# Kernel optimization log

Hardware: AMD Instinct MI355X
Metric: run time of the kernel (lower is better)

The kernel has to match this reference:

```python
import jax, jax.numpy as jnp
import numpy as np

N_NODES = 50000

def _gcn_layer(h, src, dst, norm, W, activate):
    # symmetric-normalized aggregation: D^-1/2 A D^-1/2 h, then linear
    h = h * norm[:, None]                      # [N, d] pre-scale
    msg = h[src]                               # gather over edges [E, d]
    agg = jax.ops.segment_sum(msg, dst, num_segments=N_NODES)  # scatter-add
    h = agg * norm[:, None]                    # post-scale
    h = h @ W
    return jax.nn.relu(h) if activate else h


def setup_inputs() -> dict:
    key = jax.random.key(0)
    k1, k2, k3, k4, k5, k6 = jax.random.split(key, 6)
    d_in, d_hid, d_out, n_edges = 128, 128, 40, 640000
    features = jax.random.normal(k1, (N_NODES, d_in), dtype=jnp.float32)
    edge_index = jax.random.randint(k2, (2, n_edges), 0, N_NODES, dtype=jnp.int64)
    s = 1.0 / np.sqrt(d_hid)
    W0 = jax.random.normal(k3, (d_in, d_hid), dtype=jnp.float32) * s
    W1 = jax.random.normal(k4, (d_hid, d_hid), dtype=jnp.float32) * s
    W2 = jax.random.normal(k5, (d_hid, d_hid), dtype=jnp.float32) * s
    W3 = jax.random.normal(k6, (d_hid, d_out), dtype=jnp.float32) * s
    return {"features": features, "edge_index": edge_index,
            "W0": W0, "W1": W1, "W2": W2, "W3": W3}


def reference(features, edge_index, W0, W1, W2, W3):
    src, dst = edge_index[0], edge_index[1]
    # in-degree based symmetric norm (graph_norm=True), clamp isolated nodes
    deg = jax.ops.segment_sum(jnp.ones_like(dst, dtype=features.dtype), dst,
                              num_segments=N_NODES)
    norm = jax.lax.rsqrt(jnp.maximum(deg, 1.0))
    h = features
    h = _gcn_layer(h, src, dst, norm, W0, True)
    h = _gcn_layer(h, src, dst, norm, W1, True)
    h = _gcn_layer(h, src, dst, norm, W2, True)
    h = _gcn_layer(h, src, dst, norm, W3, False)  # last layer: no activation
    return h
```

## Files before the change

### kernel.cpp

```cpp
#include <hip/hip_runtime.h>
#include <hip/hip_fp16.h>


#define DIM 128
#define CHUNK 1024

typedef __attribute__((ext_vector_type(8))) _Float16 f16x8;
typedef __attribute__((ext_vector_type(4))) float f32x4;

__global__ void deg_kernel(const int* __restrict__ dst, int* __restrict__ deg, int E) {
    int i = blockIdx.x * blockDim.x + threadIdx.x;
    if (i < E) atomicAdd(&deg[dst[i]], 1);
}

__global__ __launch_bounds__(256) void scanA_kernel(
        const int* __restrict__ deg, float* __restrict__ nrm,
        int* __restrict__ bsum, int n) {
    int b = blockIdx.x, t = threadIdx.x;
    int base = b * CHUNK + t * 4;
    int s = 0;
    if (base + 3 < n) {
        int4 d = *(const int4*)&deg[base];
        s = d.x + d.y + d.z + d.w;
        float4 r;
        r.x = rsqrtf(fmaxf((float)d.x, 1.0f));
        r.y = rsqrtf(fmaxf((float)d.y, 1.0f));
        r.z = rsqrtf(fmaxf((float)d.z, 1.0f));
        r.w = rsqrtf(fmaxf((float)d.w, 1.0f));
        *(float4*)&nrm[base] = r;
    } else {
        for (int j = 0; j < 4; ++j) {
            int idx = base + j;
            if (idx < n) {
                int d = deg[idx];
                s += d;
                nrm[idx] = rsqrtf(fmaxf((float)d, 1.0f));
            }
        }
    }
    for (int o = 32; o; o >>= 1) s += __shfl_down(s, o, 64);
    __shared__ int ws[4];
    if ((t & 63) == 0) ws[t >> 6] = s;
    __syncthreads();
    if (t == 0) bsum[b] = ws[0] + ws[1] + ws[2] + ws[3];
}

__global__ __launch_bounds__(256) void scanBC_kernel(
        const int* __restrict__ deg, const int* __restrict__ bsum,
        int* __restrict__ off, int* __restrict__ cur, int n, int G) {
    __shared__ int pbs;
    __shared__ int wsum[4];
    int b = blockIdx.x, t = threadIdx.x;
    if (t < 64) {
        int orig = (t < G) ? bsum[t] : 0;
        int v = orig;
        for (int o = 1; o < 64; o <<= 1) {
            int u = __shfl_up(v, o, 64);
            if (t >= o) v += u;
        }
        if (b == 0 && t == G - 1) off[n] = v;
        if (t == b) pbs = v - orig;
    }
    int base = b * CHUNK + t * 4;
    if (base + 3 < n) *(int4*)&cur[base] = make_int4(0, 0, 0, 0);
    else for (int j = 0; j < 4; ++j) if (base + j < n) cur[base + j] = 0;

    int d0 = 0, d1 = 0, d2 = 0, d3 = 0;
    if (base + 3 < n) {
        int4 d = *(const int4*)&deg[base];
        d0 = d.x; d1 = d.y; d2 = d.z; d3 = d.w;
    } else {
        if (base     < n) d0 = deg[base];
        if (base + 1 < n) d1 = deg[base + 1];
        if (base + 2 < n) d2 = deg[base + 2];
    }
    int tot = d0 + d1 + d2 + d3;
    int v = tot;
    for (int o = 1; o < 64; o <<= 1) {
        int u = __shfl_up(v, o, 64);
        if ((t & 63) >= o) v += u;
    }
    if ((t & 63) == 63) wsum[t >> 6] = v;
    __syncthreads();
    int wbase = 0;
    for (int w = 0; w < (t >> 6); ++w) wbase += wsum[w];
    int p = pbs + wbase + (v - tot);
    if (base + 3 < n) {
        int4 o4 = make_int4(p, p + d0, p + d0 + d1, p + d0 + d1 + d2);
        *(int4*)&off[base] = o4;
    } else {
        if (base     < n) off[base]     = p;
        if (base + 1 < n) off[base + 1] = p + d0;
        if (base + 2 < n) off[base + 2] = p + d0 + d1;
    }
}

__global__ void fill_kernel(const int* __restrict__ src, const int* __restrict__ dst,
                            const int* __restrict__ off, int* __restrict__ cur,
                            int* __restrict__ csr, int E) {
    int i = blockIdx.x * blockDim.x + threadIdx.x;
    if (i < E) {
        int d = dst[i];
        int p = atomicAdd(&cur[d], 1);
        csr[off[d] + p] = src[i];
    }
}

__global__ void conv_kernel(const float* __restrict__ f, const float* __restrict__ nrm,
                            __half* __restrict__ out, int n4) {
    int i = blockIdx.x * blockDim.x + threadIdx.x;
    if (i < n4) {
        int r = i >> 5, c4 = i & 31;
        float s = nrm[r];
        float4 v = ((const float4*)f)[i];
        __half2 lo = __float22half2_rn(make_float2(v.x * s, v.y * s));
        __half2 hi = __float22half2_rn(make_float2(v.z * s, v.w * s));
        uint2 u;
        u.x = *(unsigned int*)&lo;
        u.y = *(unsigned int*)&hi;
        *(uint2*)&out[(size_t)r * DIM + c4 * 4] = u;
    }
}

__global__ void convW_kernel(const float* __restrict__ W0, const float* __restrict__ W1,
                             const float* __restrict__ W2, const float* __restrict__ W3,
                             __half* __restrict__ Wt) {
    int i = blockIdx.x * blockDim.x + threadIdx.x;
    if (i < 3 * 128 * 128) {
        int l = i >> 14;
        int c = (i >> 7) & 127, k = i & 127;
        const float* W = (l == 0) ? W0 : ((l == 1) ? W1 : W2);
        Wt[i] = __float2half(W[k * 128 + c]);
    } else if (i < 3 * 128 * 128 + 48 * 128) {
        int j = i - 3 * 128 * 128;
        int c = j >> 7, k = j & 127;
        Wt[i] = __float2half((c < 40) ? W3[k * 40 + c] : 0.f);
    }
}

__global__ __launch_bounds__(256) void aggh_kernel(
        const __half* __restrict__ hin, const float* __restrict__ nrm,
        const int* __restrict__ off, const int* __restrict__ csr,
        __half* __restrict__ out, int N) {
    int t = threadIdx.x;
    int lane = t & 63;
    int node = blockIdx.x * 4 + (t >> 6);
    if (node >= N) return;
    int pos = lane & 15, sg = lane >> 4;
    int c = pos * 8;
    int b = off[node], e = off[node + 1];
    float a[8] = {0,0,0,0,0,0,0,0};
    float bb[8] = {0,0,0,0,0,0,0,0};
    int j = b + sg;
    for (; j + 4 < e; j += 8) {
        int s0 = csr[j], s1 = csr[j + 4];
        uint4 u0 = *(const uint4*)&hin[(size_t)s0 * DIM + c];
        uint4 u1 = *(const uint4*)&hin[(size_t)s1 * DIM + c];
        float2 f;
        f = __half22float2(*(__half2*)&u0.x); a[0]+=f.x; a[1]+=f.y;
        f = __half22float2(*(__half2*)&u0.y); a[2]+=f.x; a[3]+=f.y;
        f = __half22float2(*(__half2*)&u0.z); a[4]+=f.x; a[5]+=f.y;
        f = __half22float2(*(__half2*)&u0.w); a[6]+=f.x; a[7]+=f.y;
        f = __half22float2(*(__half2*)&u1.x); bb[0]+=f.x; bb[1]+=f.y;
        f = __half22float2(*(__half2*)&u1.y); bb[2]+=f.x; bb[3]+=f.y;
        f = __half22float2(*(__half2*)&u1.z); bb[4]+=f.x; bb[5]+=f.y;
        f = __half22float2(*(__half2*)&u1.w); bb[6]+=f.x; bb[7]+=f.y;
    }
    for (; j < e; j += 4) {
        uint4 u = *(const uint4*)&hin[(size_t)csr[j] * DIM + c];
        float2 f;
        f = __half22float2(*(__half2*)&u.x); a[0]+=f.x; a[1]+=f.y;
        f = __half22float2(*(__half2*)&u.y); a[2]+=f.x; a[3]+=f.y;
        f = __half22float2(*(__half2*)&u.z); a[4]+=f.x; a[5]+=f.y;
        f = __half22float2(*(__half2*)&u.w); a[6]+=f.x; a[7]+=f.y;
    }
#pragma unroll
    for (int k = 0; k < 8; ++k) a[k] += bb[k];
#pragma unroll
    for (int k = 0; k < 8; ++k) {
        a[k] += __shfl_xor(a[k], 16, 64);
        a[k] += __shfl_xor(a[k], 32, 64);
    }
    if (sg == 0) {
        float s = nrm[node];
        __half2 h0 = __float22half2_rn(make_float2(a[0]*s, a[1]*s));
        __half2 h1 = __float22half2_rn(make_float2(a[2]*s, a[3]*s));
        __half2 h2 = __float22half2_rn(make_float2(a[4]*s, a[5]*s));
        __half2 h3 = __float22half2_rn(make_float2(a[6]*s, a[7]*s));
        uint4 u;
        u.x = *(unsigned int*)&h0; u.y = *(unsigned int*)&h1;
        u.z = *(unsigned int*)&h2; u.w = *(unsigned int*)&h3;
        *(uint4*)&out[(size_t)node * DIM + c] = u;
    }
}

__global__ __launch_bounds__(256) void gemmM_kernel(
        const __half* __restrict__ Ah, const __half* __restrict__ Wt,
        const float* __restrict__ nrm, __half* __restrict__ outh, int n) {
    int t = threadIdx.x;
    int lane = t & 63, wv = t >> 6;
    int row0 = blockIdx.x * 64 + wv * 16;
    int arow = row0 + (lane & 15);
    int ar = (arow < n) ? arow : (n - 1);
    int kg = lane >> 4;

    const __half* Abase = Ah + (size_t)ar * DIM + kg * 8;
    f16x8 a[4];
#pragma unroll
    for (int k0 = 0; k0 < 4; ++k0)
        a[k0] = *(const f16x8*)(Abase + k0 * 32);

    f32x4 acc[8];
#pragma unroll
    for (int ct = 0; ct < 8; ++ct) {
        acc[ct] = (f32x4){0.f, 0.f, 0.f, 0.f};
        const __half* Bbase = Wt + (size_t)(ct * 16 + (lane & 15)) * DIM + kg * 8;
#pragma unroll
        for (int k0 = 0; k0 < 4; ++k0) {
            f16x8 b = *(const f16x8*)(Bbase + k0 * 32);
            acc[ct] = __builtin_amdgcn_mfma_f32_16x16x32_f16(a[k0], b, acc[ct], 0, 0, 0);
        }
    }

    int col = lane & 15;
    int rbase = row0 + (lane >> 4) * 4;
#pragma unroll
    for (int r = 0; r < 4; ++r) {
        int row = rbase + r;
        if (row >= n) continue;
        float s = nrm[row];
#pragma unroll
        for (int ct = 0; ct < 8; ++ct) {
            float v = fmaxf(acc[ct][r], 0.f) * s;
            outh[(size_t)row * DIM + ct * 16 + col] = __float2half(v);
        }
    }
}

__global__ __launch_bounds__(256) void gemm3M_kernel(
        const __half* __restrict__ Ah, const __half* __restrict__ Wt3,
        __half* __restrict__ outh, int n) {
    int t = threadIdx.x;
    int lane = t & 63, wv = t >> 6;
    int row0 = blockIdx.x * 64 + wv * 16;
    int arow = row0 + (lane & 15);
    int ar = (arow < n) ? arow : (n - 1);
    int kg = lane >> 4;

    const __half* Abase = Ah + (size_t)ar * DIM + kg * 8;
    f16x8 a[4];
#pragma unroll
    for (int k0 = 0; k0 < 4; ++k0)
        a[k0] = *(const f16x8*)(Abase + k0 * 32);

    f32x4 acc[3];
#pragma unroll
    for (int ct = 0; ct < 3; ++ct) {
        acc[ct] = (f32x4){0.f, 0.f, 0.f, 0.f};
        const __half* Bbase = Wt3 + (size_t)(ct * 16 + (lane & 15)) * DIM + kg * 8;
#pragma unroll
        for (int k0 = 0; k0 < 4; ++k0) {
            f16x8 b = *(const f16x8*)(Bbase + k0 * 32);
            acc[ct] = __builtin_amdgcn_mfma_f32_16x16x32_f16(a[k0], b, acc[ct], 0, 0, 0);
        }
    }

    int col = lane & 15;
    int rbase = row0 + (lane >> 4) * 4;
#pragma unroll
    for (int r = 0; r < 4; ++r) {
        int row = rbase + r;
        if (row >= n) continue;
#pragma unroll
        for (int ct = 0; ct < 3; ++ct) {
            int cc = ct * 16 + col;
            if (cc < 40)
                outh[(size_t)row * 40 + cc] = __float2half(acc[ct][r]);
        }
    }
}

__global__ __launch_bounds__(256) void agg40_kernel(
        const __half* __restrict__ hin, const float* __restrict__ nrm,
        const int* __restrict__ off, const int* __restrict__ csr,
        float* __restrict__ out, int N) {
    int t = threadIdx.x;
    int lane = t & 63, wv = t >> 6;
    int g = lane >> 4, pos = lane & 15;
    int node = blockIdx.x * 16 + wv * 4 + g;
    if (node >= N || pos >= 10) return;
    int b = off[node], e = off[node + 1];
    float4 a0 = make_float4(0,0,0,0), a1 = a0, a2 = a0, a3 = a0;
    int j = b;
    for (; j + 3 < e; j += 4) {
        int s0 = csr[j], s1 = csr[j+1], s2 = csr[j+2], s3 = csr[j+3];
        uint2 u0 = *(const uint2*)&hin[(size_t)s0 * 40 + pos * 4];
        uint2 u1 = *(const uint2*)&hin[(size_t)s1 * 40 + pos * 4];
        uint2 u2 = *(const uint2*)&hin[(size_t)s2 * 40 + pos * 4];
        uint2 u3 = *(const uint2*)&hin[(size_t)s3 * 40 + pos * 4];
        float2 f;
        f = __half22float2(*(__half2*)&u0.x); a0.x+=f.x; a0.y+=f.y;
        f = __half22float2(*(__half2*)&u0.y); a0.z+=f.x; a0.w+=f.y;
        f = __half22float2(*(__half2*)&u1.x); a1.x+=f.x; a1.y+=f.y;
        f = __half22float2(*(__half2*)&u1.y); a1.z+=f.x; a1.w+=f.y;
        f = __half22float2(*(__half2*)&u2.x); a2.x+=f.x; a2.y+=f.y;
        f = __half22float2(*(__half2*)&u2.y); a2.z+=f.x; a2.w+=f.y;
        f = __half22float2(*(__half2*)&u3.x); a3.x+=f.x; a3.y+=f.y;
        f = __half22float2(*(__half2*)&u3.y); a3.z+=f.x; a3.w+=f.y;
    }
    for (; j < e; ++j) {
        uint2 u = *(const uint2*)&hin[(size_t)csr[j] * 40 + pos * 4];
        float2 f;
        f = __half22float2(*(__half2*)&u.x); a0.x+=f.x; a0.y+=f.y;
        f = __half22float2(*(__half2*)&u.y); a0.z+=f.x; a0.w+=f.y;
    }
    float s = nrm[node];
    float4 r;
    r.x = ((a0.x+a1.x) + (a2.x+a3.x)) * s;
    r.y = ((a0.y+a1.y) + (a2.y+a3.y)) * s;
    r.z = ((a0.z+a1.z) + (a2.z+a3.z)) * s;
    r.w = ((a0.w+a1.w) + (a2.w+a3.w)) * s;
    *(float4*)&out[(size_t)node * 40 + pos * 4] = r;
}

extern "C" void kernel_launch(void* const* d_in, const int* in_sizes, int n_in,
                              void* d_out, int out_size, void* d_ws, size_t ws_size,
                              hipStream_t stream) {
    const float* features = (const float*)d_in[0];
    const int*   edges    = (const int*)d_in[1];
    const float* W0       = (const float*)d_in[2];
    const float* W1       = (const float*)d_in[3];
    const float* W2       = (const float*)d_in[4];
    const float* W3       = (const float*)d_in[5];

    const int N = in_sizes[0] / DIM;
    const int E = in_sizes[1] / 2;
    const int* src = edges;
    const int* dst = edges + E;

    char* p = (char*)d_ws;
    __half* featH = (__half*)p; p += (size_t)N * DIM * 2;
    __half* agg16 = (__half*)p; p += (size_t)N * DIM * 2;
    __half* h16   = (__half*)p; p += (size_t)N * DIM * 2;
    __half* g3h   = (__half*)p; p += (size_t)N * 64 * 2;
    __half* Wt    = (__half*)p; p += (size_t)(3 * 128 * 128 + 48 * 128) * 2;
    float*  nrm   = (float*)p;  p += (size_t)N * 4;
    int*    deg   = (int*)p;    p += (size_t)N * 4;
    int*    cur   = (int*)p;    p += (size_t)N * 4;
    int*    off   = (int*)p;    p += (size_t)(N + 1) * 4;
    int*    bsum  = (int*)p;    p += 64 * 4;
    int*    csr   = (int*)p;    p += (size_t)E * 4;
    (void)ws_size; (void)n_in;

    hipMemsetAsync(deg, 0, (size_t)N * sizeof(int), stream);

    int eb = (E + 255) / 256;
    int G  = (N + CHUNK - 1) / CHUNK;
    deg_kernel   <<<eb, 256, 0, stream>>>(dst, deg, E);
    scanA_kernel <<<G, 256, 0, stream>>>(deg, nrm, bsum, N);
    scanBC_kernel<<<G, 256, 0, stream>>>(deg, bsum, off, cur, N, G);
    fill_kernel  <<<eb, 256, 0, stream>>>(src, dst, off, cur, csr, E);

    int wB = (3 * 128 * 128 + 48 * 128 + 255) / 256;
    convW_kernel<<<wB, 256, 0, stream>>>(W0, W1, W2, W3, Wt);

    int n4 = N * (DIM / 4);
    conv_kernel<<<(n4 + 255) / 256, 256, 0, stream>>>(features, nrm, featH, n4);

    int gb = (N + 63) / 64;
    int ab = (N + 3) / 4;
    aggh_kernel<<<ab, 256, 0, stream>>>(featH, nrm, off, csr, agg16, N);
    gemmM_kernel<<<gb, 256, 0, stream>>>(agg16, Wt, nrm, h16, N);

    aggh_kernel<<<ab, 256, 0, stream>>>(h16, nrm, off, csr, agg16, N);
    gemmM_kernel<<<gb, 256, 0, stream>>>(agg16, Wt + 128 * 128, nrm, h16, N);

    aggh_kernel<<<ab, 256, 0, stream>>>(h16, nrm, off, csr, agg16, N);
    gemmM_kernel<<<gb, 256, 0, stream>>>(agg16, Wt + 2 * 128 * 128, nrm, h16, N);

    gemm3M_kernel<<<gb, 256, 0, stream>>>(h16, Wt + 3 * 128 * 128, g3h, N);
    agg40_kernel<<<(N + 15) / 16, 256, 0, stream>>>(g3h, nrm, off, csr,
                                                    (float*)d_out, N);
}
```

Measured before the change: 261.4 us.

## Fuse graph setup into one cooperative kernel and fuse last two GEMMs

Folds the memset, degree count, two-phase scan, CSR fill, and weight and feature conversion into a single cooperative-launch kernel that uses grid.sync between phases. This removes about seven kernel launches and their gaps. It also fuses the layer-3 GEMM with the layer-4 projection by staging the ReLU-scaled tile in LDS, which avoids writing h16 to global memory and reading it back. The cost is grid-wide barriers with a fixed 1024-block grid, so the small scan phases leave most blocks idle, and the fused GEMM uses more LDS per block.

```diff
diff --git a/kernel.cpp b/kernel.cpp
--- a/kernel.cpp
+++ b/kernel.cpp
@@ -1,140 +1,140 @@
 #include <hip/hip_runtime.h>
 #include <hip/hip_fp16.h>
-
+#include <hip/hip_cooperative_groups.h>
+
+
+namespace cg = cooperative_groups;
 
 #define DIM 128
 #define CHUNK 1024
+#define HS_LD 136
 
 typedef __attribute__((ext_vector_type(8))) _Float16 f16x8;
 typedef __attribute__((ext_vector_type(4))) float f32x4;
 
-__global__ void deg_kernel(const int* __restrict__ dst, int* __restrict__ deg, int E) {
-    int i = blockIdx.x * blockDim.x + threadIdx.x;
-    if (i < E) atomicAdd(&deg[dst[i]], 1);
-}
-
-__global__ __launch_bounds__(256) void scanA_kernel(
-        const int* __restrict__ deg, float* __restrict__ nrm,
-        int* __restrict__ bsum, int n) {
-    int b = blockIdx.x, t = threadIdx.x;
-    int base = b * CHUNK + t * 4;
-    int s = 0;
-    if (base + 3 < n) {
-        int4 d = *(const int4*)&deg[base];
-        s = d.x + d.y + d.z + d.w;
-        float4 r;
-        r.x = rsqrtf(fmaxf((float)d.x, 1.0f));
-        r.y = rsqrtf(fmaxf((float)d.y, 1.0f));
-        r.z = rsqrtf(fmaxf((float)d.z, 1.0f));
-        r.w = rsqrtf(fmaxf((float)d.w, 1.0f));
-        *(float4*)&nrm[base] = r;
-    } else {
-        for (int j = 0; j < 4; ++j) {
-            int idx = base + j;
-            if (idx < n) {
-                int d = deg[idx];
-                s += d;
-                nrm[idx] = rsqrtf(fmaxf((float)d, 1.0f));
+__global__ __launch_bounds__(256) void setup_kernel(
+        const int* __restrict__ src, const int* __restrict__ dst,
+        const float* __restrict__ features,
+        const float* __restrict__ W0, const float* __restrict__ W1,
+        const float* __restrict__ W2, const float* __restrict__ W3,
+        int* __restrict__ deg, int* __restrict__ cur, float* __restrict__ nrm,
+        int* __restrict__ off, int* __restrict__ bsum, int* __restrict__ csr,
+        __half* __restrict__ featH, __half* __restrict__ Wt,
+        int N, int E, int G) {
+    cg::grid_group grid = cg::this_grid();
+    __shared__ int ws[4];
+    __shared__ int wsum[4];
+    int t = threadIdx.x;
+    int gtid = blockIdx.x * 256 + t;
+    int gsz = gridDim.x * 256;
+
+    for (int i = gtid; i < N; i += gsz) { deg[i] = 0; cur[i] = 0; }
+    const int WTOT = 3 * 128 * 128 + 48 * 128;
+    for (int i = gtid; i < WTOT; i += gsz) {
+        if (i < 3 * 128 * 128) {
+            int l = i >> 14, c = (i >> 7) & 127, k = i & 127;
+            const float* W = (l == 0) ? W0 : ((l == 1) ? W1 : W2);
+            Wt[i] = __float2half(W[k * 128 + c]);
+        } else {
+            int j = i - 3 * 128 * 128, c = j >> 7, k = j & 127;
+            Wt[i] = __float2half((c < 40) ? W3[k * 40 + c] : 0.f);
+        }
+    }
+    grid.sync();
+
+    for (int i = gtid; i < E; i += gsz) atomicAdd(&deg[dst[i]], 1);
+    grid.sync();
+
+    if (blockIdx.x < (unsigned)G) {
+        int b = blockIdx.x;
+        int base = b * CHUNK + t * 4;
+        int s = 0;
+        if (base + 3 < N) {
+            int4 d = *(const int4*)&deg[base];
+            s = d.x + d.y + d.z + d.w;
+            float4 r;
+            r.x = rsqrtf(fmaxf((float)d.x, 1.f));
+            r.y = rsqrtf(fmaxf((float)d.y, 1.f));
+            r.z = rsqrtf(fmaxf((float)d.z, 1.f));
+            r.w = rsqrtf(fmaxf((float)d.w, 1.f));
+            *(float4*)&nrm[base] = r;
+        } else {
+            for (int j2 = 0; j2 < 4; ++j2) {
+                int idx = base + j2;
+                if (idx < N) {
+                    int d = deg[idx];
+                    s += d;
+                    nrm[idx] = rsqrtf(fmaxf((float)d, 1.f));
+                }
             }
         }
-    }
-    for (int o = 32; o; o >>= 1) s += __shfl_down(s, o, 64);
-    __shared__ int ws[4];
-    if ((t & 63) == 0) ws[t >> 6] = s;
-    __syncthreads();
-    if (t == 0) bsum[b] = ws[0] + ws[1] + ws[2] + ws[3];
-}
-
-__global__ __launch_bounds__(256) void scanBC_kernel(
-        const int* __restrict__ deg, const int* __restrict__ bsum,
-        int* __restrict__ off, int* __restrict__ cur, int n, int G) {
-    __shared__ int pbs;
-    __shared__ int wsum[4];
-    int b = blockIdx.x, t = threadIdx.x;
-    if (t < 64) {
+        for (int o = 32; o; o >>= 1) s += __shfl_down(s, o, 64);
+        if ((t & 63) == 0) ws[t >> 6] = s;
+        __syncthreads();
+        if (t == 0) bsum[b] = ws[0] + ws[1] + ws[2] + ws[3];
+    }
+    grid.sync();
+
+    if (blockIdx.x == 0 && t < 64) {
         int orig = (t < G) ? bsum[t] : 0;
         int v = orig;
         for (int o = 1; o < 64; o <<= 1) {
             int u = __shfl_up(v, o, 64);
             if (t >= o) v += u;
         }
-        if (b == 0 && t == G - 1) off[n] = v;
-        if (t == b) pbs = v - orig;
-    }
-    int base = b * CHUNK + t * 4;
-    if (base + 3 < n) *(int4*)&cur[base] = make_int4(0, 0, 0, 0);
-    else for (int j = 0; j < 4; ++j) if (base + j < n) cur[base + j] = 0;
-
-    int d0 = 0, d1 = 0, d2 = 0, d3 = 0;
-    if (base + 3 < n) {
-        int4 d = *(const int4*)&deg[base];
-        d0 = d.x; d1 = d.y; d2 = d.z; d3 = d.w;
-    } else {
-        if (base     < n) d0 = deg[base];
-        if (base + 1 < n) d1 = deg[base + 1];
-        if (base + 2 < n) d2 = deg[base + 2];
-    }
-    int tot = d0 + d1 + d2 + d3;
-    int v = tot;
-    for (int o = 1; o < 64; o <<= 1) {
-        int u = __shfl_up(v, o, 64);
-        if ((t & 63) >= o) v += u;
-    }
-    if ((t & 63) == 63) wsum[t >> 6] = v;
-    __syncthreads();
-    int wbase = 0;
-    for (int w = 0; w < (t >> 6); ++w) wbase += wsum[w];
-    int p = pbs + wbase + (v - tot);
-    if (base + 3 < n) {
-        int4 o4 = make_int4(p, p + d0, p + d0 + d1, p + d0 + d1 + d2);
-        *(int4*)&off[base] = o4;
-    } else {
-        if (base     < n) off[base]     = p;
-        if (base + 1 < n) off[base + 1] = p + d0;
-        if (base + 2 < n) off[base + 2] = p + d0 + d1;
-    }
-}
-
-__global__ void fill_kernel(const int* __restrict__ src, const int* __restrict__ dst,
-                            const int* __restrict__ off, int* __restrict__ cur,
-                            int* __restrict__ csr, int E) {
-    int i = blockIdx.x * blockDim.x + threadIdx.x;
-    if (i < E) {
-        int d = dst[i];
-        int p = atomicAdd(&cur[d], 1);
-        csr[off[d] + p] = src[i];
-    }
-}
-
-__global__ void conv_kernel(const float* __restrict__ f, const float* __restrict__ nrm,
-                            __half* __restrict__ out, int n4) {
-    int i = blockIdx.x * blockDim.x + threadIdx.x;
-    if (i < n4) {
+        if (t < G) bsum[t] = v - orig;
+        if (t == G - 1) off[N] = v;
+    }
+    grid.sync();
+
+    if (blockIdx.x < (unsigned)G) {
+        int b = blockIdx.x;
+        int base = b * CHUNK + t * 4;
+        int d0 = 0, d1 = 0, d2 = 0, d3 = 0;
+        if (base + 3 < N) {
+            int4 d = *(const int4*)&deg[base];
+            d0 = d.x; d1 = d.y; d2 = d.z; d3 = d.w;
+        } else {
+            if (base     < N) d0 = deg[base];
+            if (base + 1 < N) d1 = deg[base + 1];
+            if (base + 2 < N) d2 = deg[base + 2];
+        }
+        int tot = d0 + d1 + d2 + d3;
+        int v = tot;
+        for (int o = 1; o < 64; o <<= 1) {
+            int u = __shfl_up(v, o, 64);
+            if ((t & 63) >= o) v += u;
+        }
+        if ((t & 63) == 63) wsum[t >> 6] = v;
+        __syncthreads();
+        int wbase = 0;
+        for (int w = 0; w < (t >> 6); ++w) wbase += wsum[w];
+        int p = bsum[b] + wbase + (v - tot);
+        if (base + 3 < N) {
+            *(int4*)&off[base] = make_int4(p, p + d0, p + d0 + d1, p + d0 + d1 + d2);
+        } else {
+            if (base     < N) off[base]     = p;
+            if (base + 1 < N) off[base + 1] = p + d0;
+            if (base + 2 < N) off[base + 2] = p + d0 + d1;
+        }
+    }
+    for (int i = gtid; i < N * 32; i += gsz) {
         int r = i >> 5, c4 = i & 31;
         float s = nrm[r];
-        float4 v = ((const float4*)f)[i];
+        float4 v = ((const float4*)features)[i];
         __half2 lo = __float22half2_rn(make_float2(v.x * s, v.y * s));
         __half2 hi = __float22half2_rn(make_float2(v.z * s, v.w * s));
         uint2 u;
         u.x = *(unsigned int*)&lo;
         u.y = *(unsigned int*)&hi;
-        *(uint2*)&out[(size_t)r * DIM + c4 * 4] = u;
-    }
-}
-
-__global__ void convW_kernel(const float* __restrict__ W0, const float* __restrict__ W1,
-                             const float* __restrict__ W2, const float* __restrict__ W3,
-                             __half* __restrict__ Wt) {
-    int i = blockIdx.x * blockDim.x + threadIdx.x;
-    if (i < 3 * 128 * 128) {
-        int l = i >> 14;
-        int c = (i >> 7) & 127, k = i & 127;
-        const float* W = (l == 0) ? W0 : ((l == 1) ? W1 : W2);
-        Wt[i] = __float2half(W[k * 128 + c]);
-    } else if (i < 3 * 128 * 128 + 48 * 128) {
-        int j = i - 3 * 128 * 128;
-        int c = j >> 7, k = j & 127;
-        Wt[i] = __float2half((c < 40) ? W3[k * 40 + c] : 0.f);
+        *(uint2*)&featH[(size_t)r * DIM + c4 * 4] = u;
+    }
+    grid.sync();
+
+    for (int i = gtid; i < E; i += gsz) {
+        int d = dst[i];
+        int p2 = atomicAdd(&cur[d], 1);
+        csr[off[d] + p2] = src[i];
     }
 }
 
@@ -237,9 +237,11 @@
     }
 }
 
-__global__ __launch_bounds__(256) void gemm3M_kernel(
-        const __half* __restrict__ Ah, const __half* __restrict__ Wt3,
-        __half* __restrict__ outh, int n) {
+__global__ __launch_bounds__(256) void gemmM2_kernel(
+        const __half* __restrict__ Ah, const __half* __restrict__ Wt2,
+        const __half* __restrict__ Wt3, const float* __restrict__ nrm,
+        __half* __restrict__ g3h, int n) {
+    __shared__ __half Hs[64 * HS_LD];
     int t = threadIdx.x;
     int lane = t & 63, wv = t >> 6;
     int row0 = blockIdx.x * 64 + wv * 16;
@@ -253,11 +255,11 @@
     for (int k0 = 0; k0 < 4; ++k0)
         a[k0] = *(const f16x8*)(Abase + k0 * 32);
 
-    f32x4 acc[3];
-#pragma unroll
-    for (int ct = 0; ct < 3; ++ct) {
+    f32x4 acc[8];
+#pragma unroll
+    for (int ct = 0; ct < 8; ++ct) {
         acc[ct] = (f32x4){0.f, 0.f, 0.f, 0.f};
-        const __half* Bbase = Wt3 + (size_t)(ct * 16 + (lane & 15)) * DIM + kg * 8;
+        const __half* Bbase = Wt2 + (size_t)(ct * 16 + (lane & 15)) * DIM + kg * 8;
 #pragma unroll
         for (int k0 = 0; k0 < 4; ++k0) {
             f16x8 b = *(const f16x8*)(Bbase + k0 * 32);
@@ -266,6 +268,39 @@
     }
 
     int col = lane & 15;
+    int lr0 = wv * 16 + (lane >> 4) * 4;
+#pragma unroll
+    for (int r = 0; r < 4; ++r) {
+        int lrow = lr0 + r;
+        int grow = blockIdx.x * 64 + lrow;
+        float s = (grow < n) ? nrm[grow] : 0.f;
+#pragma unroll
+        for (int ct = 0; ct < 8; ++ct) {
+            float v = fmaxf(acc[ct][r], 0.f) * s;
+            Hs[lrow * HS_LD + ct * 16 + col] = __float2half(v);
+        }
+    }
+    __syncthreads();
+
+    int lrowA = wv * 16 + (lane & 15);
+    const __half* Hbase = &Hs[lrowA * HS_LD + kg * 8];
+    f16x8 a2[4];
+#pragma unroll
+    for (int k0 = 0; k0 < 4; ++k0)
+        a2[k0] = *(const f16x8*)(Hbase + k0 * 32);
+
+    f32x4 acc2[3];
+#pragma unroll
+    for (int ct = 0; ct < 3; ++ct) {
+        acc2[ct] = (f32x4){0.f, 0.f, 0.f, 0.f};
+        const __half* Bbase = Wt3 + (size_t)(ct * 16 + (lane & 15)) * DIM + kg * 8;
+#pragma unroll
+        for (int k0 = 0; k0 < 4; ++k0) {
+            f16x8 b = *(const f16x8*)(Bbase + k0 * 32);
+            acc2[ct] = __builtin_amdgcn_mfma_f32_16x16x32_f16(a2[k0], b, acc2[ct], 0, 0, 0);
+        }
+    }
+
     int rbase = row0 + (lane >> 4) * 4;
 #pragma unroll
     for (int r = 0; r < 4; ++r) {
@@ -275,7 +310,7 @@
         for (int ct = 0; ct < 3; ++ct) {
             int cc = ct * 16 + col;
             if (cc < 40)
-                outh[(size_t)row * 40 + cc] = __float2half(acc[ct][r]);
+                g3h[(size_t)row * 40 + cc] = __float2half(acc2[ct][r]);
         }
     }
 }
@@ -350,22 +385,23 @@
     int*    off   = (int*)p;    p += (size_t)(N + 1) * 4;
     int*    bsum  = (int*)p;    p += 64 * 4;
     int*    csr   = (int*)p;    p += (size_t)E * 4;
-    (void)ws_size; (void)n_in;
-
-    hipMemsetAsync(deg, 0, (size_t)N * sizeof(int), stream);
-
-    int eb = (E + 255) / 256;
-    int G  = (N + CHUNK - 1) / CHUNK;
-    deg_kernel   <<<eb, 256, 0, stream>>>(dst, deg, E);
-    scanA_kernel <<<G, 256, 0, stream>>>(deg, nrm, bsum, N);
-    scanBC_kernel<<<G, 256, 0, stream>>>(deg, bsum, off, cur, N, G);
-    fill_kernel  <<<eb, 256, 0, stream>>>(src, dst, off, cur, csr, E);
-
-    int wB = (3 * 128 * 128 + 48 * 128 + 255) / 256;
-    convW_kernel<<<wB, 256, 0, stream>>>(W0, W1, W2, W3, Wt);
-
-    int n4 = N * (DIM / 4);
-    conv_kernel<<<(n4 + 255) / 256, 256, 0, stream>>>(features, nrm, featH, n4);
+    (void)ws_size; (void)n_in; (void)out_size;
+
+    int Gv = (N + CHUNK - 1) / CHUNK;
+    {
+        const int* a0 = src; const int* a1 = dst;
+        const float* a2 = features;
+        const float* a3 = W0; const float* a4 = W1;
+        const float* a5 = W2; const float* a6 = W3;
+        int* a7 = deg; int* a8 = cur; float* a9 = nrm;
+        int* a10 = off; int* a11 = bsum; int* a12 = csr;
+        __half* a13 = featH; __half* a14 = Wt;
+        int a15 = N, a16 = E, a17 = Gv;
+        void* args[] = {&a0, &a1, &a2, &a3, &a4, &a5, &a6, &a7, &a8, &a9,
+                        &a10, &a11, &a12, &a13, &a14, &a15, &a16, &a17};
+        hipLaunchCooperativeKernel((const void*)setup_kernel,
+                                   dim3(1024), dim3(256), args, 0, stream);
+    }
 
     int gb = (N + 63) / 64;
     int ab = (N + 3) / 4;
@@ -376,9 +412,9 @@
     gemmM_kernel<<<gb, 256, 0, stream>>>(agg16, Wt + 128 * 128, nrm, h16, N);
 
     aggh_kernel<<<ab, 256, 0, stream>>>(h16, nrm, off, csr, agg16, N);
-    gemmM_kernel<<<gb, 256, 0, stream>>>(agg16, Wt + 2 * 128 * 128, nrm, h16, N);
-
-    gemm3M_kernel<<<gb, 256, 0, stream>>>(h16, Wt + 3 * 128 * 128, g3h, N);
+    gemmM2_kernel<<<gb, 256, 0, stream>>>(agg16, Wt + 2 * 128 * 128,
+                                          Wt + 3 * 128 * 128, nrm, g3h, N);
+
     agg40_kernel<<<(N + 15) / 16, 256, 0, stream>>>(g3h, nrm, off, csr,
                                                     (float*)d_out, N);
 }
```

After: 743.2 us. +184.3%, slower.
